# Kernel tuning notes

Hardware: AMD Instinct MI355X
Metric: run time of the kernel (lower is better)

## Reference

```python
import jax, jax.numpy as jnp
import numpy as np

H = 8          # num_heads
FOCUS = 3      # focusing_factor
EPS = 1e-6


def _disagreement(h):
    # h: [B, Hn, N, d]; mean of pairwise cosine-sim matrix with diagonal zeroed
    B, Hn, N, d = h.shape
    hn = h / jnp.maximum(jnp.linalg.norm(h, axis=-1, keepdims=True), 1e-12)
    sim_sum = jnp.sum(jnp.einsum('bhnd,bhmd->bhnm', hn, hn))
    diag_sum = jnp.sum(hn * hn)  # diagonal entries of the sim matrix
    return (sim_sum - diag_sum) / (B * Hn * N * N)


def setup_inputs() -> dict:
    key = jax.random.key(0)
    ks = jax.random.split(key, 10)
    B, N, C, K = 4, 1024, 512, 10
    s = 0.02
    return {
        'Q': jax.random.normal(ks[0], (B, N, C), jnp.float32),
        'adj_mat': jax.random.randint(ks[1], (B, N, K), 0, N),
        'Wq': jax.random.normal(ks[2], (C, C), jnp.float32) * s,
        'bq': jnp.zeros((C,), jnp.float32),
        'Wk': jax.random.normal(ks[3], (C, C), jnp.float32) * s,
        'bk': jnp.zeros((C,), jnp.float32),
        'Wv': jax.random.normal(ks[4], (C, C), jnp.float32) * s,
        'bv': jnp.zeros((C,), jnp.float32),
        'scale_p': jnp.zeros((1, 1, C), jnp.float32),  # torch init: zeros
        'Wconv': jax.random.normal(ks[5], (C, C, K + 1), jnp.float32) * s,
        'bconv': jnp.zeros((C,), jnp.float32),
        'W2': jax.random.normal(ks[6], (C, C), jnp.float32) * s,
        'b2': jnp.zeros((C,), jnp.float32),
        'ln_g': jnp.ones((C,), jnp.float32),
        'ln_b': jnp.zeros((C,), jnp.float32),
        'Wo': jax.random.normal(ks[7], (C, C), jnp.float32) * s,
        'bo': jnp.zeros((C,), jnp.float32),
    }


def _forward(Q, adj_mat, Wq, bq, Wk, bk, Wv, bv, scale_p, Wconv, bconv,
             W2, b2, ln_g, ln_b, Wo, bo):
    B, N, C = Q.shape
    d = C // H
    q = Q @ Wq + bq
    k = Q @ Wk + bk
    v = Q @ Wv + bv

    # LocalFeatureExtractor on v: gather K neighbors, conv over (channel, K+1) window
    neigh = v[jnp.arange(B)[:, None, None], adj_mat]          # [B,N,K,C]
    feats = jnp.concatenate([v[:, :, None, :], neigh], axis=2)  # [B,N,K+1,C]
    conv = jnp.einsum('bntc,oct->bno', feats, Wconv) + bconv   # full-window conv1d
    x_local = conv @ W2 + b2                                   # [B,N,C]

    # kernelized q/k with softplus scale and focused normalization
    q = jax.nn.relu(q) + EPS
    k = jax.nn.relu(k) + EPS
    scale = jax.nn.softplus(scale_p)
    q = q / scale
    k = k / scale

    def focus(x):
        n = jnp.linalg.norm(x, axis=-1, keepdims=True)
        return (x / (n + EPS)) ** FOCUS * n

    q = focus(q)
    k = focus(k)

    q = q.reshape(B, N, H, d).transpose(0, 2, 1, 3)
    k = k.reshape(B, N, H, d).transpose(0, 2, 1, 3)
    vh = v.reshape(B, N, H, d).transpose(0, 2, 1, 3)

    # linear attention: z normalization and kv summarization
    z = 1.0 / (jnp.einsum('bhnd,bhd->bhn', q, k.mean(axis=2)) + EPS)  # [B,H,N]
    kv = jnp.einsum('bhnd,bhne->bhde', k, vh) / N                     # [B,H,d,d]
    x = jnp.einsum('bhnd,bhde->bhne', q, kv) * z[..., None]           # [B,H,N,d]

    loss_local = _disagreement(vh)
    loss_kv = _disagreement(kv)

    x = x.transpose(0, 2, 1, 3).reshape(B, N, C) + x_local
    x4 = x.reshape(B, H, N, d)  # raw memory reinterpretation, matches torch .reshape
    loss_out = _disagreement(x4)
    loss = (loss_local + loss_out + loss_kv) / 3.0
    x = x4.reshape(B, N, C)

    # out_proj: LayerNorm then Linear
    mu = x.mean(axis=-1, keepdims=True)
    var = jnp.mean((x - mu) ** 2, axis=-1, keepdims=True)
    xn = (x - mu) / jnp.sqrt(var + 1e-5) * ln_g + ln_b
    out = xn @ Wo + bo
    return out, loss


def reference(Q, adj_mat, Wq, bq, Wk, bk, Wv, bv, scale_p, Wconv, bconv,
              W2, b2, ln_g, ln_b, Wo, bo):
    return _forward(Q, adj_mat, Wq, bq, Wk, bk, Wv, bv, scale_p, Wconv, bconv,
                    W2, b2, ln_g, ln_b, Wo, bo)
```

## Files before the change

### kernel.cpp

```cpp
#include <hip/hip_runtime.h>
#include <math.h>

#define TOK_TOTAL 4096
#define KNB 10
#define MATE 2097152

typedef __attribute__((ext_vector_type(8))) short short8;
typedef __attribute__((ext_vector_type(4))) float floatx4;
typedef unsigned short ushort;

__device__ __forceinline__ floatx4 mfma16(short8 a, short8 b, floatx4 c) {
  return __builtin_amdgcn_mfma_f32_16x16x32_bf16(a, b, c, 0, 0, 0);
}

__device__ __forceinline__ ushort f2bf(float f) {
  union { float f; unsigned int u; } x; x.f = f;
  unsigned int r = x.u + 0x7fffu + ((x.u >> 16) & 1u);
  return (ushort)(r >> 16);
}

__device__ __forceinline__ float bf2f(ushort u) {
  union { unsigned int u; float f; } x; x.u = ((unsigned int)u) << 16;
  return x.f;
}

__device__ __forceinline__ float lane_bcast(float v, int l) {
  union { float f; int i; } x; x.f = v;
  x.i = __builtin_amdgcn_readlane(x.i, l);
  return x.f;
}

__device__ __forceinline__ void glds16(const ushort* g, ushort* l) {
  __builtin_amdgcn_global_load_lds((const __attribute__((address_space(1))) void*)g,
                                   (__attribute__((address_space(3))) void*)l, 16, 0, 0);
}

__device__ __forceinline__ float wave_reduce_sum(float v) {
#pragma unroll
  for (int m = 32; m >= 1; m >>= 1) v += __shfl_xor(v, m, 64);
  return v;
}

__device__ __forceinline__ float block_reduce_sum_256(float v, float* red) {
  v = wave_reduce_sum(v);
  __syncthreads();
  if ((threadIdx.x & 63) == 0) red[threadIdx.x >> 6] = v;
  __syncthreads();
  return red[0] + red[1] + red[2] + red[3];
}

__global__ __launch_bounds__(256) void prep_kernel(const float* __restrict__ Wq,
                                                   const float* __restrict__ Wk,
                                                   const float* __restrict__ Wv,
                                                   const float* __restrict__ W2p,
                                                   const float* __restrict__ Wo,
                                                   const float* __restrict__ Wconv,
                                                   const float* __restrict__ Q,
                                                   const float* __restrict__ bq,
                                                   const float* __restrict__ bk,
                                                   const float* __restrict__ bv,
                                                   ushort* __restrict__ WT,
                                                   ushort* __restrict__ BcY,
                                                   float* __restrict__ biasqkv,
                                                   ushort* __restrict__ Qb) {
  int blk = blockIdx.x;
  if (blk < 1280) {
    __shared__ float tile[32][33];
    int zz = blk >> 8, rem = blk & 255;
    const float* W = (zz == 0) ? Wq : (zz == 1) ? Wk : (zz == 2) ? Wv
                     : (zz == 3) ? W2p : Wo;
    ushort* Wt = WT + (size_t)zz * 262144;
    int n0 = (rem & 15) * 32, k0 = (rem >> 4) * 32;
    int tx = threadIdx.x & 31, ty = threadIdx.x >> 5;
#pragma unroll
    for (int i = 0; i < 32; i += 8)
      tile[ty + i][tx] = W[(size_t)(k0 + ty + i) * 512 + n0 + tx];
    __syncthreads();
#pragma unroll
    for (int i = 0; i < 32; i += 8)
      Wt[(size_t)(n0 + ty + i) * 512 + k0 + tx] = f2bf(tile[tx][ty + i]);
  } else if (blk < 2304) {
    int i = (blk - 1280) * 256 + threadIdx.x;
    const float* src = Wconv + (size_t)i * 11;
    int o = i >> 9, c = i & 511;
#pragma unroll
    for (int t = 0; t < 11; ++t)
      BcY[(((size_t)(t * 512 + o)) << 9) + c] = f2bf(src[t]);
  } else if (blk == 2304) {
    for (int i = threadIdx.x; i < 1536; i += 256)
      biasqkv[i] = (i < 512) ? bq[i] : ((i < 1024) ? bk[i - 512] : bv[i - 1024]);
  } else {
    int i = (blk - 2305) * 256 + threadIdx.x;
    float4 v = *(const float4*)(Q + (size_t)i * 4);
    Qb[(size_t)i * 4 + 0] = f2bf(v.x);
    Qb[(size_t)i * 4 + 1] = f2bf(v.y);
    Qb[(size_t)i * 4 + 2] = f2bf(v.z);
    Qb[(size_t)i * 4 + 3] = f2bf(v.w);
  }
}

__global__ __launch_bounds__(256, 2) void gemm128(const ushort* __restrict__ A,
                                                  const ushort* __restrict__ Bt,
                                                  ushort* __restrict__ Cb,
                                                  int Ktot, int Ncols) {
  __shared__ __align__(16) ushort As[2][8192];
  __shared__ __align__(16) ushort Bs[2][8192];
  int tid = threadIdx.x, w = tid >> 6, lane = tid & 63;
  int lm = lane & 15, kq = lane >> 4;
  int row0 = blockIdx.y * 128, col0 = blockIdx.x * 128;
  int wm = w >> 1, wn = w & 1;

  bool isA = (w < 2);
  const ushort* gs[8];
  int go[8];
#pragma unroll
  for (int i = 0; i < 8; ++i) {
    int slab = (w & 1) * 4 + (i >> 1);
    int j = i & 1;
    const ushort* base = isA ? (A + (size_t)(row0 + slab * 16 + lm) * Ktot)
                             : (Bt + (size_t)(col0 + slab * 16 + lm) * Ktot);
    gs[i] = base + j * 32 + kq * 8;
    go[i] = slab * 1024 + j * 512;
  }

  floatx4 acc[4][4];
#pragma unroll
  for (int i = 0; i < 4; ++i)
#pragma unroll
    for (int j = 0; j < 4; ++j)
#pragma unroll
      for (int e = 0; e < 4; ++e) acc[i][j][e] = 0.f;

#pragma unroll
  for (int i = 0; i < 8; ++i)
    glds16(gs[i], (isA ? As[0] : Bs[0]) + go[i]);

  int nsteps = Ktot >> 6;
  for (int s = 0; s < nsteps; ++s) {
    int buf = s & 1;
    __syncthreads();
    if (s + 1 < nsteps) {
      int koff = (s + 1) << 6;
      ushort* dst = (isA ? As[buf ^ 1] : Bs[buf ^ 1]);
#pragma unroll
      for (int i = 0; i < 8; ++i) glds16(gs[i] + koff, dst + go[i]);
    }
#pragma unroll
    for (int j = 0; j < 2; ++j) {
      short8 a[4], b[4];
#pragma unroll
      for (int mt = 0; mt < 4; ++mt)
        a[mt] = *(const short8*)(&As[buf][(wm * 4 + mt) * 1024 + j * 512 + lane * 8]);
#pragma unroll
      for (int nt = 0; nt < 4; ++nt)
        b[nt] = *(const short8*)(&Bs[buf][(wn * 4 + nt) * 1024 + j * 512 + lane * 8]);
#pragma unroll
      for (int mt = 0; mt < 4; ++mt)
#pragma unroll
        for (int nt = 0; nt < 4; ++nt)
          acc[mt][nt] = mfma16(a[mt], b[nt], acc[mt][nt]);
    }
  }

#pragma unroll
  for (int mt = 0; mt < 4; ++mt) {
#pragma unroll
    for (int nt = 0; nt < 4; ++nt) {
      int col = col0 + wn * 64 + nt * 16 + lm;
#pragma unroll
      for (int r = 0; r < 4; ++r) {
        int row = row0 + wm * 64 + mt * 16 + kq * 4 + r;
        Cb[(size_t)row * Ncols + col] = f2bf(acc[mt][nt][r]);
      }
    }
  }
}

__global__ __launch_bounds__(256, 2) void gemm128_qkv(const ushort* __restrict__ A,
                                                      const ushort* __restrict__ Bt,
                                                      const float* __restrict__ bias,
                                                      float* __restrict__ outf,
                                                      ushort* __restrict__ vb) {
  __shared__ __align__(16) ushort As[2][8192];
  __shared__ __align__(16) ushort Bs[2][8192];
  int tid = threadIdx.x, w = tid >> 6, lane = tid & 63;
  int lm = lane & 15, kq = lane >> 4;
  int row0 = blockIdx.y * 128, col0 = blockIdx.x * 128;
  int wm = w >> 1, wn = w & 1;

  bool isA = (w < 2);
  const ushort* gs[8];
  int go[8];
#pragma unroll
  for (int i = 0; i < 8; ++i) {
    int slab = (w & 1) * 4 + (i >> 1);
    int j = i & 1;
    const ushort* base = isA ? (A + (size_t)(row0 + slab * 16 + lm) * 512)
                             : (Bt + (size_t)(col0 + slab * 16 + lm) * 512);
    gs[i] = base + j * 32 + kq * 8;
    go[i] = slab * 1024 + j * 512;
  }

  floatx4 acc[4][4];
#pragma unroll
  for (int i = 0; i < 4; ++i)
#pragma unroll
    for (int j = 0; j < 4; ++j)
#pragma unroll
      for (int e = 0; e < 4; ++e) acc[i][j][e] = 0.f;

#pragma unroll
  for (int i = 0; i < 8; ++i)
    glds16(gs[i], (isA ? As[0] : Bs[0]) + go[i]);

  for (int s = 0; s < 8; ++s) {
    int buf = s & 1;
    __syncthreads();
    if (s + 1 < 8) {
      int koff = (s + 1) << 6;
      ushort* dst = (isA ? As[buf ^ 1] : Bs[buf ^ 1]);
#pragma unroll
      for (int i = 0; i < 8; ++i) glds16(gs[i] + koff, dst + go[i]);
    }
#pragma unroll
    for (int j = 0; j < 2; ++j) {
      short8 a[4], b[4];
#pragma unroll
      for (int mt = 0; mt < 4; ++mt)
        a[mt] = *(const short8*)(&As[buf][(wm * 4 + mt) * 1024 + j * 512 + lane * 8]);
#pragma unroll
      for (int nt = 0; nt < 4; ++nt)
        b[nt] = *(const short8*)(&Bs[buf][(wn * 4 + nt) * 1024 + j * 512 + lane * 8]);
#pragma unroll
      for (int mt = 0; mt < 4; ++mt)
#pragma unroll
        for (int nt = 0; nt < 4; ++nt)
          acc[mt][nt] = mfma16(a[mt], b[nt], acc[mt][nt]);
    }
  }

#pragma unroll
  for (int mt = 0; mt < 4; ++mt) {
#pragma unroll
    for (int nt = 0; nt < 4; ++nt) {
      int col = col0 + wn * 64 + nt * 16 + lm;
      int mat = col >> 9, cc = col & 511;
      float bs = bias[col];
#pragma unroll
      for (int r = 0; r < 4; ++r) {
        int row = row0 + wm * 64 + mt * 16 + kq * 4 + r;
        float val = acc[mt][nt][r] + bs;
        size_t idx = (size_t)row * 512 + cc;
        outf[(size_t)mat * MATE + idx] = val;
        if (mat == 2) vb[idx] = f2bf(val);
      }
    }
  }
}

__global__ __launch_bounds__(256) void gather_add_bias(const ushort* __restrict__ Y,
                                                       const int* __restrict__ adj,
                                                       const float* __restrict__ bias,
                                                       ushort* __restrict__ convb) {
  int n = (blockIdx.x << 1) + (threadIdx.x >> 7);
  int b10 = (n >> 10) << 10;
  int o = (threadIdx.x & 127) << 2;
  float4 bs = *(const float4*)(bias + o);
  float a0 = bs.x, a1 = bs.y, a2 = bs.z, a3 = bs.w;
#pragma unroll
  for (int t = 0; t < 11; ++t) {
    int src = (t == 0) ? n : (b10 + adj[(size_t)n * KNB + (t - 1)]);
    const ushort* p = Y + (size_t)src * 5632 + (size_t)t * 512 + o;
    uint2 u = *(const uint2*)p;
    a0 += bf2f((ushort)(u.x & 0xffff));
    a1 += bf2f((ushort)(u.x >> 16));
    a2 += bf2f((ushort)(u.y & 0xffff));
    a3 += bf2f((ushort)(u.y >> 16));
  }
  uint2 w;
  w.x = (unsigned)f2bf(a0) | ((unsigned)f2bf(a1) << 16);
  w.y = (unsigned)f2bf(a2) | ((unsigned)f2bf(a3) << 16);
  *(uint2*)(convb + (size_t)n * 512 + o) = w;
}

__global__ __launch_bounds__(256) void gather_add(const ushort* __restrict__ Y,
                                                  const int* __restrict__ adj,
                                                  float* __restrict__ convf,
                                                  int t0, int ntaps, int ncols) {
  int n = blockIdx.x;
  int b10 = (n >> 10) << 10;
  int o = threadIdx.x * 2;
  float a0 = 0.f, a1 = 0.f;
  for (int t = t0; t < t0 + ntaps; ++t) {
    int src = (t == 0) ? n : (b10 + adj[(size_t)n * KNB + (t - 1)]);
    const ushort* p = Y + (size_t)src * ncols + (size_t)(t - t0) * 512 + o;
    a0 += bf2f(p[0]);
    a1 += bf2f(p[1]);
  }
  convf[(size_t)n * 512 + o] += a0;
  convf[(size_t)n * 512 + o + 1] += a1;
}

__global__ __launch_bounds__(256) void convbias_cast(const float* __restrict__ cf,
                                                     const float* __restrict__ bias,
                                                     ushort* __restrict__ cb) {
  int i = blockIdx.x * 256 + threadIdx.x;
  float4 v = *(const float4*)(cf + (size_t)i * 4);
  int c = (i * 4) & 511;
  cb[(size_t)i * 4 + 0] = f2bf(v.x + bias[c + 0]);
  cb[(size_t)i * 4 + 1] = f2bf(v.y + bias[c + 1]);
  cb[(size_t)i * 4 + 2] = f2bf(v.z + bias[c + 2]);
  cb[(size_t)i * 4 + 3] = f2bf(v.w + bias[c + 3]);
}

__global__ __launch_bounds__(256) void gemm64(const ushort* __restrict__ A,
                                              const ushort* __restrict__ Bt,
                                              const float* __restrict__ bias,
                                              float* __restrict__ Cf,
                                              ushort* __restrict__ Cb,
                                              int Ktot) {
  __shared__ __align__(16) ushort As[2][4096];
  __shared__ __align__(16) ushort Bs[2][4096];
  int tid = threadIdx.x, w = tid >> 6, lane = tid & 63;
  int lm = lane & 15, kq = lane >> 4;
  int row0 = blockIdx.y * 64, col0 = blockIdx.x * 64;
  int wm = w >> 1, wn = w & 1;

  const ushort* gsrc[4];
  int goff[4];
  bool isA = (w < 2);
#pragma unroll
  for (int i = 0; i < 4; ++i) {
    int l = w * 4 + i, t, j;
    const ushort* base;
    if (l < 8) { t = l >> 1; j = l & 1; base = A + (size_t)(row0 + t * 16 + lm) * Ktot; }
    else { int lb = l - 8; t = lb >> 1; j = lb & 1; base = Bt + (size_t)(col0 + t * 16 + lm) * Ktot; }
    gsrc[i] = base + j * 32 + kq * 8;
    goff[i] = t * 1024 + j * 512;
  }

  floatx4 acc[2][2];
#pragma unroll
  for (int i = 0; i < 2; ++i)
#pragma unroll
    for (int j = 0; j < 2; ++j)
#pragma unroll
      for (int e = 0; e < 4; ++e) acc[i][j][e] = 0.f;

#pragma unroll
  for (int i = 0; i < 4; ++i)
    glds16(gsrc[i], (isA ? As[0] : Bs[0]) + goff[i]);

  int nsteps = Ktot >> 6;
  for (int s = 0; s < nsteps; ++s) {
    int buf = s & 1;
    __syncthreads();
    if (s + 1 < nsteps) {
      int koff = (s + 1) << 6;
      ushort* dst = (isA ? As[buf ^ 1] : Bs[buf ^ 1]);
#pragma unroll
      for (int i = 0; i < 4; ++i) glds16(gsrc[i] + koff, dst + goff[i]);
    }
#pragma unroll
    for (int j = 0; j < 2; ++j) {
      short8 a0 = *(const short8*)(&As[buf][(wm * 2 + 0) * 1024 + j * 512 + lane * 8]);
      short8 a1 = *(const short8*)(&As[buf][(wm * 2 + 1) * 1024 + j * 512 + lane * 8]);
      short8 b0 = *(const short8*)(&Bs[buf][(wn * 2 + 0) * 1024 + j * 512 + lane * 8]);
      short8 b1 = *(const short8*)(&Bs[buf][(wn * 2 + 1) * 1024 + j * 512 + lane * 8]);
      acc[0][0] = mfma16(a0, b0, acc[0][0]);
      acc[0][1] = mfma16(a0, b1, acc[0][1]);
      acc[1][0] = mfma16(a1, b0, acc[1][0]);
      acc[1][1] = mfma16(a1, b1, acc[1][1]);
    }
  }

  int colb = col0 + wn * 32;
  int rowb = row0 + wm * 32 + kq * 4;
#pragma unroll
  for (int mt = 0; mt < 2; ++mt) {
#pragma unroll
    for (int nt = 0; nt < 2; ++nt) {
      int col = colb + nt * 16 + lm;
      float bs = bias[col];
#pragma unroll
      for (int r = 0; r < 4; ++r) {
        int row = rowb + mt * 16 + r;
        float val = acc[mt][nt][r] + bs;
        size_t idx = (size_t)row * 512 + col;
        if (Cf) Cf[idx] = val;
        if (Cb) Cb[idx] = f2bf(val);
      }
    }
  }
}

__global__ __launch_bounds__(256) void focus_kernel(float* __restrict__ x,
                                                    const float* __restrict__ scale_p) {
  __shared__ float red[4];
  int row = blockIdx.x;
  float* p = x + (size_t)row * 512;
  int tid = threadIdx.x;
  float sp0 = scale_p[tid], sp1 = scale_p[tid + 256];
  float sc0 = sp0 > 20.f ? sp0 : log1pf(expf(sp0));
  float sc1 = sp1 > 20.f ? sp1 : log1pf(expf(sp1));
  float v0 = (fmaxf(p[tid], 0.f) + 1e-6f) / sc0;
  float v1 = (fmaxf(p[tid + 256], 0.f) + 1e-6f) / sc1;
  float tot = block_reduce_sum_256(v0 * v0 + v1 * v1, red);
  float n = sqrtf(tot);
  float np = n + 1e-6f;
  float f = n / (np * np * np);
  p[tid] = v0 * v0 * v0 * f;
  p[tid + 256] = v1 * v1 * v1 * f;
}

__global__ __launch_bounds__(256) void kv_kernel(const float* __restrict__ kf,
                                                 const float* __restrict__ v,
                                                 float* __restrict__ kv,
                                                 float* __restrict__ Sacc,
                                                 float* __restrict__ Dacc,
                                                 float* __restrict__ kmean) {
  __shared__ float Ks[16][64];
  __shared__ float Vs[16][64];
  __shared__ float Spart[64];
  __shared__ float Kpart[64];
  __shared__ float Dpart;
  int bh = blockIdx.x >> 3, chunk = blockIdx.x & 7;
  int b = bh >> 3, h = bh & 7;
  int tid = threadIdx.x;
  int lr = tid >> 4, lc = (tid & 15) << 2;
  int tx = tid & 15, ty = tid >> 4;
  if (tid < 64) { Spart[tid] = 0.f; Kpart[tid] = 0.f; }
  if (tid == 0) Dpart = 0.f;
  __syncthreads();
  const float* kbase = kf + (size_t)b * 524288 + h * 64 + (size_t)chunk * 128 * 512;
  const float* vbase = v + (size_t)b * 524288 + h * 64 + (size_t)chunk * 128 * 512;
  float acc[4][4] = {};
  float Sloc[4] = {0.f, 0.f, 0.f, 0.f};
  float Kloc[4] = {0.f, 0.f, 0.f, 0.f};
  float Dloc = 0.f;
  for (int n0 = 0; n0 < 128; n0 += 16) {
    float4 ke = *(const float4*)(kbase + (size_t)(n0 + lr) * 512 + lc);
    *(float4*)(&Ks[lr][lc]) = ke;
    Kloc[0] += ke.x; Kloc[1] += ke.y; Kloc[2] += ke.z; Kloc[3] += ke.w;
    float4 ve = *(const float4*)(vbase + (size_t)(n0 + lr) * 512 + lc);
    *(float4*)(&Vs[lr][lc]) = ve;
    __syncthreads();
    float sq = ve.x * ve.x + ve.y * ve.y + ve.z * ve.z + ve.w * ve.w;
#pragma unroll
    for (int m = 1; m < 16; m <<= 1) sq += __shfl_xor(sq, m, 64);
    float cn = fmaxf(sqrtf(sq), 1e-12f);
    Sloc[0] += ve.x / cn; Sloc[1] += ve.y / cn;
    Sloc[2] += ve.z / cn; Sloc[3] += ve.w / cn;
    if ((tid & 15) == 0) Dloc += sq / (cn * cn);
#pragma unroll
    for (int kk = 0; kk < 16; ++kk) {
      float a[4], bb[4];
#pragma unroll
      for (int i = 0; i < 4; ++i) a[i] = Ks[kk][ty * 4 + i];
#pragma unroll
      for (int j = 0; j < 4; ++j) bb[j] = Vs[kk][tx * 4 + j];
#pragma unroll
      for (int i = 0; i < 4; ++i)
#pragma unroll
        for (int j = 0; j < 4; ++j) acc[i][j] += a[i] * bb[j];
    }
    __syncthreads();
  }
#pragma unroll
  for (int i = 0; i < 4; ++i)
#pragma unroll
    for (int j = 0; j < 4; ++j)
      atomicAdd(&kv[(size_t)bh * 4096 + (ty * 4 + i) * 64 + tx * 4 + j],
                acc[i][j] * (1.f / 1024.f));
#pragma unroll
  for (int i = 0; i < 4; ++i) {
    atomicAdd(&Spart[lc + i], Sloc[i]);
    atomicAdd(&Kpart[lc + i], Kloc[i]);
  }
  if ((tid & 15) == 0) atomicAdd(&Dpart, Dloc);
  __syncthreads();
  if (tid < 64) {
    atomicAdd(&Sacc[bh * 64 + tid], Spart[tid]);
    atomicAdd(&kmean[b * 512 + h * 64 + tid], Kpart[tid] * (1.f / 1024.f));
  }
  if (tid == 64) atomicAdd(&Dacc[bh], Dpart);
}

__global__ __launch_bounds__(512, 4) void attn_ln_kernel(const float* __restrict__ qf,
                                                         const float* __restrict__ kvf,
                                                         const float* __restrict__ kmean,
                                                         const float* __restrict__ x_local,
                                                         const float* __restrict__ g,
                                                         const float* __restrict__ bp,
                                                         ushort* __restrict__ xn,
                                                         float* __restrict__ Sacc,
                                                         float* __restrict__ Dacc,
                                                         float* __restrict__ Skv,
                                                         float* __restrict__ Dkv) {
  __shared__ __align__(16) ushort kvs[32768];
  __shared__ float red[16];
  __shared__ float Sl[8][64];
  __shared__ float Dl[8];
  int r0 = blockIdx.x << 3;
  int b = r0 >> 10;
  int c = threadIdx.x, wv = c >> 6, lane = c & 63;
  const float4* kvg = (const float4*)(kvf + (size_t)b * 32768);
#pragma unroll
  for (int i = 0; i < 16; ++i) {
    float4 kvv = kvg[c + i * 512];
    int o = (c + i * 512) << 2;
    kvs[o + 0] = f2bf(kvv.x); kvs[o + 1] = f2bf(kvv.y);
    kvs[o + 2] = f2bf(kvv.z); kvs[o + 3] = f2bf(kvv.w);
  }
  float kmr = kmean[b * 512 + c];
  float gr = g[c], bpr = bp[c];
  __syncthreads();
  unsigned int kvr[32];
#pragma unroll
  for (int i = 0; i < 32; ++i) {
    unsigned int lo = kvs[wv * 4096 + (2 * i) * 64 + lane];
    unsigned int hi = kvs[wv * 4096 + (2 * i + 1) * 64 + lane];
    kvr[i] = lo | (hi << 16);
  }
  float Sreg = 0.f, Dreg = 0.f;
  for (int r = 0; r < 8; ++r) {
    int row = r0 + r;
    float qv = qf[(size_t)row * 512 + c];
    float xl = x_local[(size_t)row * 512 + c];
    float zd = wave_reduce_sum(qv * kmr);
    float zz = 1.f / (zd + 1e-6f);
    float s = 0.f;
#pragma unroll
    for (int i = 0; i < 32; ++i) {
      union { unsigned int u; float f; } lo, hi;
      lo.u = kvr[i] << 16;
      hi.u = kvr[i] & 0xffff0000u;
      s += lane_bcast(qv, 2 * i) * lo.f;
      s += lane_bcast(qv, 2 * i + 1) * hi.f;
    }
    float xv = s * zz + xl;
    float s1 = wave_reduce_sum(xv);
    float s2 = wave_reduce_sum(xv * xv);
    if (lane == 0) { red[wv] = s1; red[8 + wv] = s2; }
    __syncthreads();
    float tsum = red[0] + red[1] + red[2] + red[3] + red[4] + red[5] + red[6] + red[7];
    float tsq = red[8] + red[9] + red[10] + red[11] + red[12] + red[13] + red[14] + red[15];
    __syncthreads();
    float mu = tsum * (1.f / 512.f);
    float var = tsq * (1.f / 512.f) - mu * mu;
    float inv = rsqrtf(fmaxf(var, 0.f) + 1e-5f);
    xn[(size_t)row * 512 + c] = f2bf((xv - mu) * inv * gr + bpr);
    float norm = fmaxf(sqrtf(s2), 1e-12f);
    Sreg += xv / norm;
    Dreg += s2 / (norm * norm);
  }
  Sl[wv][lane] = Sreg;
  if (lane == 0) Dl[wv] = Dreg;
  __syncthreads();
  int gx = b * 8 + ((r0 & 1023) >> 7);
  if (c < 64) {
    float ssum = 0.f;
#pragma unroll
    for (int ww = 0; ww < 8; ++ww) ssum += Sl[ww][c];
    atomicAdd(&Sacc[gx * 64 + c], ssum);
  } else if (c == 64) {
    float dsum = 0.f;
#pragma unroll
    for (int ww = 0; ww < 8; ++ww) dsum += Dl[ww];
    atomicAdd(&Dacc[gx], dsum);
  }
  if ((blockIdx.x & 127) == 0) {
    float S2 = 0.f, D2 = 0.f;
#pragma unroll
    for (int i = 0; i < 32; ++i) {
      union { unsigned int u; float f; } lo, hi;
      lo.u = kvr[i] << 16;
      hi.u = kvr[i] & 0xffff0000u;
      float sq = wave_reduce_sum(lo.f * lo.f);
      float nrm = fmaxf(sqrtf(sq), 1e-12f);
      float hn = lo.f / nrm;
      S2 += hn; D2 += hn * hn;
      sq = wave_reduce_sum(hi.f * hi.f);
      nrm = fmaxf(sqrtf(sq), 1e-12f);
      hn = hi.f / nrm;
      S2 += hn; D2 += hn * hn;
    }
    float dt = wave_reduce_sum(D2);
    atomicAdd(&Skv[(b * 8 + wv) * 64 + lane], S2);
    if (lane == 0) atomicAdd(&Dkv[b * 8 + wv], dt);
  }
}

__global__ __launch_bounds__(64) void disagree_final_all(const float* __restrict__ Sall,
                                                         const float* __restrict__ Dall,
                                                         float s0, float s1, float s2,
                                                         float* __restrict__ loss) {
  int set = blockIdx.x >> 5, gg = blockIdx.x & 31;
  int l = threadIdx.x;
  float sv = Sall[set * 2048 + gg * 64 + l];
  float sim = wave_reduce_sum(sv * sv);
  if (l == 0) {
    float scale = (set == 0) ? s0 : (set == 1) ? s1 : s2;
    atomicAdd(loss, (sim - Dall[set * 32 + gg]) * scale);
  }
}

extern "C" void kernel_launch(void* const* d_in, const int* in_sizes, int n_in,
                              void* d_out, int out_size, void* d_ws, size_t ws_size,
                              hipStream_t stream) {
  const float* Q       = (const float*)d_in[0];
  const int*   adj     = (const int*)d_in[1];
  const float* Wq      = (const float*)d_in[2];
  const float* bq      = (const float*)d_in[3];
  const float* Wk      = (const float*)d_in[4];
  const float* bk      = (const float*)d_in[5];
  const float* Wv      = (const float*)d_in[6];
  const float* bv      = (const float*)d_in[7];
  const float* scale_p = (const float*)d_in[8];
  const float* Wconv   = (const float*)d_in[9];
  const float* bconv   = (const float*)d_in[10];
  const float* W2      = (const float*)d_in[11];
  const float* b2      = (const float*)d_in[12];
  const float* ln_g    = (const float*)d_in[13];
  const float* ln_b    = (const float*)d_in[14];
  const float* Wo      = (const float*)d_in[15];
  const float* bo      = (const float*)d_in[16];

  float* out = (float*)d_out;
  float* loss_slot = out + MATE;

  float* ws = (float*)d_ws;
  float* q0      = ws;
  float* k0      = q0 + MATE;
  float* v       = k0 + MATE;
  float* x_local = v + MATE;
  float* convf   = x_local + MATE;
  ushort* Qb    = (ushort*)(convf + MATE);
  ushort* vb    = Qb + MATE;
  ushort* convb = vb + MATE;
  ushort* xnb   = convb + MATE;
  ushort* WqT   = xnb + MATE;
  ushort* W2T   = WqT + 3 * 262144;
  ushort* WoT   = W2T + 262144;
  ushort* BcY   = WoT + 262144;
  float* biasqkv = (float*)(BcY + 5632 * 512);
  float* kmean = biasqkv + 1536;
  float* kvbuf = kmean + 2048;
  float* Sv    = kvbuf + 131072;
  float* Skv   = Sv + 2048;
  float* Sx    = Skv + 2048;
  float* Dv    = Sx + 2048;
  float* Dkv   = Dv + 32;
  float* Dx    = Dkv + 32;
  float* ytail = Dx + 32;
  ushort* Ybf  = (ushort*)ytail;

  size_t used_floats = (size_t)(ytail - ws);
  size_t avail_floats = (ws_size / 4 > used_floats) ? (ws_size / 4 - used_floats) : 0;
  int TC = (int)(avail_floats / (MATE / 2));
  if (TC < 1) TC = 1;
  if (TC > 11) TC = 11;

  hipMemsetAsync(loss_slot, 0, sizeof(float), stream);
  hipMemsetAsync(kmean, 0, (2048 + 131072 + 3 * 2048 + 96) * sizeof(float), stream);

  prep_kernel<<<4353, 256, 0, stream>>>(Wq, Wk, Wv, W2, Wo, Wconv, Q,
                                        bq, bk, bv, WqT, BcY, biasqkv, Qb);

  gemm128_qkv<<<dim3(12, 32), 256, 0, stream>>>(Qb, WqT, biasqkv, q0, vb);

  if (TC >= 11) {
    gemm128<<<dim3(44, 32), 256, 0, stream>>>(vb, BcY, Ybf, 512, 5632);
    gather_add_bias<<<2048, 256, 0, stream>>>(Ybf, adj, bconv, convb);
  } else {
    hipMemsetAsync(convf, 0, MATE * sizeof(float), stream);
    for (int t0 = 0; t0 < 11; t0 += TC) {
      int nt = (11 - t0 < TC) ? (11 - t0) : TC;
      int ncols = nt * 512;
      gemm128<<<dim3(ncols / 128, 32), 256, 0, stream>>>(
          vb, BcY + (size_t)(t0 * 512) * 512, Ybf, 512, ncols);
      gather_add<<<4096, 256, 0, stream>>>(Ybf, adj, convf, t0, nt, ncols);
    }
    convbias_cast<<<2048, 256, 0, stream>>>(convf, bconv, convb);
  }

  gemm64<<<dim3(8, 64), 256, 0, stream>>>(convb, W2T, b2, x_local, nullptr, 512);

  focus_kernel<<<2 * TOK_TOTAL, 256, 0, stream>>>(q0, scale_p);

  kv_kernel<<<256, 256, 0, stream>>>(k0, v, kvbuf, Sv, Dv, kmean);

  attn_ln_kernel<<<512, 512, 0, stream>>>(q0, kvbuf, kmean, x_local,
                                          ln_g, ln_b, xnb, Sx, Dx, Skv, Dkv);

  disagree_final_all<<<96, 64, 0, stream>>>(Sv, Dv,
                                            1.f / (33554432.f * 3.f),
                                            1.f / (131072.f * 3.f),
                                            1.f / (33554432.f * 3.f), loss_slot);

  gemm64<<<dim3(8, 64), 256, 0, stream>>>(xnb, WoT, bo, out, nullptr, 512);
}
```

Measured before the change: 295.8 us.

## Fold W2 into conv weights and fuse neighbor gather into a split-K GEMM

```diff
diff --git a/kernel.cpp b/kernel.cpp
--- a/kernel.cpp
+++ b/kernel.cpp
@@ -17,11 +17,6 @@
   union { float f; unsigned int u; } x; x.f = f;
   unsigned int r = x.u + 0x7fffu + ((x.u >> 16) & 1u);
   return (ushort)(r >> 16);
-}
-
-__device__ __forceinline__ float bf2f(ushort u) {
-  union { unsigned int u; float f; } x; x.u = ((unsigned int)u) << 16;
-  return x.f;
 }
 
 __device__ __forceinline__ float lane_bcast(float v, int l) {
@@ -59,9 +54,12 @@
                                                    const float* __restrict__ bq,
                                                    const float* __restrict__ bk,
                                                    const float* __restrict__ bv,
+                                                   const float* __restrict__ bconv,
+                                                   const float* __restrict__ b2,
                                                    ushort* __restrict__ WT,
-                                                   ushort* __restrict__ BcY,
+                                                   ushort* __restrict__ WcT,
                                                    float* __restrict__ biasqkv,
+                                                   float* __restrict__ bias2f,
                                                    ushort* __restrict__ Qb) {
   int blk = blockIdx.x;
   if (blk < 1280) {
@@ -81,16 +79,27 @@
       Wt[(size_t)(n0 + ty + i) * 512 + k0 + tx] = f2bf(tile[tx][ty + i]);
   } else if (blk < 2304) {
     int i = (blk - 1280) * 256 + threadIdx.x;
-    const float* src = Wconv + (size_t)i * 11;
-    int o = i >> 9, c = i & 511;
+    int o1 = i & 511, c = i >> 9;
+    const float* src = Wconv + ((size_t)o1 * 512 + c) * 11;
 #pragma unroll
     for (int t = 0; t < 11; ++t)
-      BcY[(((size_t)(t * 512 + o)) << 9) + c] = f2bf(src[t]);
+      WcT[(((size_t)(t * 512 + c)) << 9) + o1] = f2bf(src[t]);
   } else if (blk == 2304) {
     for (int i = threadIdx.x; i < 1536; i += 256)
       biasqkv[i] = (i < 512) ? bq[i] : ((i < 1024) ? bk[i - 512] : bv[i - 1024]);
+  } else if (blk < 2307) {
+    __shared__ float bc[512];
+    int tid = threadIdx.x;
+    bc[tid] = bconv[tid];
+    bc[tid + 256] = bconv[tid + 256];
+    __syncthreads();
+    int o = (blk - 2305) * 256 + tid;
+    float s = b2[o];
+#pragma unroll 4
+    for (int o1 = 0; o1 < 512; ++o1) s += bc[o1] * W2p[(size_t)o1 * 512 + o];
+    bias2f[o] = s;
   } else {
-    int i = (blk - 2305) * 256 + threadIdx.x;
+    int i = (blk - 2307) * 256 + threadIdx.x;
     float4 v = *(const float4*)(Q + (size_t)i * 4);
     Qb[(size_t)i * 4 + 0] = f2bf(v.x);
     Qb[(size_t)i * 4 + 1] = f2bf(v.y);
@@ -258,59 +267,127 @@
   }
 }
 
-__global__ __launch_bounds__(256) void gather_add_bias(const ushort* __restrict__ Y,
-                                                       const int* __restrict__ adj,
-                                                       const float* __restrict__ bias,
-                                                       ushort* __restrict__ convb) {
-  int n = (blockIdx.x << 1) + (threadIdx.x >> 7);
-  int b10 = (n >> 10) << 10;
-  int o = (threadIdx.x & 127) << 2;
-  float4 bs = *(const float4*)(bias + o);
-  float a0 = bs.x, a1 = bs.y, a2 = bs.z, a3 = bs.w;
-#pragma unroll
-  for (int t = 0; t < 11; ++t) {
-    int src = (t == 0) ? n : (b10 + adj[(size_t)n * KNB + (t - 1)]);
-    const ushort* p = Y + (size_t)src * 5632 + (size_t)t * 512 + o;
-    uint2 u = *(const uint2*)p;
-    a0 += bf2f((ushort)(u.x & 0xffff));
-    a1 += bf2f((ushort)(u.x >> 16));
-    a2 += bf2f((ushort)(u.y & 0xffff));
-    a3 += bf2f((ushort)(u.y >> 16));
-  }
-  uint2 w;
-  w.x = (unsigned)f2bf(a0) | ((unsigned)f2bf(a1) << 16);
-  w.y = (unsigned)f2bf(a2) | ((unsigned)f2bf(a3) << 16);
-  *(uint2*)(convb + (size_t)n * 512 + o) = w;
-}
-
-__global__ __launch_bounds__(256) void gather_add(const ushort* __restrict__ Y,
-                                                  const int* __restrict__ adj,
-                                                  float* __restrict__ convf,
-                                                  int t0, int ntaps, int ncols) {
-  int n = blockIdx.x;
-  int b10 = (n >> 10) << 10;
-  int o = threadIdx.x * 2;
-  float a0 = 0.f, a1 = 0.f;
-  for (int t = t0; t < t0 + ntaps; ++t) {
-    int src = (t == 0) ? n : (b10 + adj[(size_t)n * KNB + (t - 1)]);
-    const ushort* p = Y + (size_t)src * ncols + (size_t)(t - t0) * 512 + o;
-    a0 += bf2f(p[0]);
-    a1 += bf2f(p[1]);
-  }
-  convf[(size_t)n * 512 + o] += a0;
-  convf[(size_t)n * 512 + o + 1] += a1;
-}
-
-__global__ __launch_bounds__(256) void convbias_cast(const float* __restrict__ cf,
-                                                     const float* __restrict__ bias,
-                                                     ushort* __restrict__ cb) {
-  int i = blockIdx.x * 256 + threadIdx.x;
-  float4 v = *(const float4*)(cf + (size_t)i * 4);
-  int c = (i * 4) & 511;
-  cb[(size_t)i * 4 + 0] = f2bf(v.x + bias[c + 0]);
-  cb[(size_t)i * 4 + 1] = f2bf(v.y + bias[c + 1]);
-  cb[(size_t)i * 4 + 2] = f2bf(v.z + bias[c + 2]);
-  cb[(size_t)i * 4 + 3] = f2bf(v.w + bias[c + 3]);
+__global__ __launch_bounds__(256) void gemm_gather(const ushort* __restrict__ A,
+                                                   const ushort* __restrict__ Bt,
+                                                   const int* __restrict__ adj,
+                                                   const float* __restrict__ bias2,
+                                                   float* __restrict__ xpart) {
+  __shared__ __align__(16) ushort As[2][8192];
+  __shared__ __align__(16) ushort Bs[2][8192];
+  int tid = threadIdx.x, w = tid >> 6, lane = tid & 63;
+  int lm = lane & 15, kq = lane >> 4;
+  int row0 = blockIdx.y * 128, col0 = blockIdx.x * 128;
+  int z = blockIdx.z;
+  int kbase = z * 2816;
+  int wm = w >> 1, wn = w & 1;
+  bool isA = (w < 2);
+
+  int go[8];
+#pragma unroll
+  for (int i = 0; i < 8; ++i) {
+    int slab = (w & 1) * 4 + (i >> 1);
+    go[i] = slab * 1024 + (i & 1) * 512;
+  }
+
+  int rowi[4], b10v[4], srcnext[4];
+  const ushort* gsB[8];
+  if (isA) {
+    int tap0 = kbase >> 9;
+    int t0 = tap0 ? tap0 : 1;
+#pragma unroll
+    for (int p = 0; p < 4; ++p) {
+      int r = row0 + ((w & 1) * 4 + p) * 16 + lm;
+      rowi[p] = r;
+      b10v[p] = (r >> 10) << 10;
+      int av = b10v[p] + adj[r * KNB + t0 - 1];
+      srcnext[p] = tap0 ? av : r;
+    }
+  } else {
+#pragma unroll
+    for (int i = 0; i < 8; ++i) {
+      int slab = (w & 1) * 4 + (i >> 1);
+      gsB[i] = Bt + (size_t)(col0 + slab * 16 + lm) * 5632 + kbase + (i & 1) * 32 + kq * 8;
+    }
+  }
+
+  floatx4 acc[4][4];
+#pragma unroll
+  for (int i = 0; i < 4; ++i)
+#pragma unroll
+    for (int j = 0; j < 4; ++j)
+#pragma unroll
+      for (int e = 0; e < 4; ++e) acc[i][j][e] = 0.f;
+
+  {
+    int koff = kbase & 511;
+    if (isA) {
+#pragma unroll
+      for (int i = 0; i < 8; ++i)
+        glds16(A + (size_t)srcnext[i >> 1] * 512 + koff + (i & 1) * 32 + kq * 8,
+               As[0] + go[i]);
+    } else {
+#pragma unroll
+      for (int i = 0; i < 8; ++i) glds16(gsB[i], Bs[0] + go[i]);
+    }
+  }
+
+  const int nsteps = 44;
+  for (int s = 0; s < nsteps; ++s) {
+    int buf = s & 1;
+    __syncthreads();
+    if (s + 1 < nsteps) {
+      if (isA) {
+        int koff = (kbase + (s + 1) * 64) & 511;
+        ushort* dst = As[buf ^ 1];
+#pragma unroll
+        for (int i = 0; i < 8; ++i)
+          glds16(A + (size_t)srcnext[i >> 1] * 512 + koff + (i & 1) * 32 + kq * 8,
+                 dst + go[i]);
+        int s2 = (s + 2 < nsteps) ? s + 2 : nsteps - 1;
+        int tap2 = (kbase + s2 * 64) >> 9;
+        int t2 = tap2 ? tap2 : 1;
+#pragma unroll
+        for (int p = 0; p < 4; ++p) {
+          int av = b10v[p] + adj[rowi[p] * KNB + t2 - 1];
+          srcnext[p] = tap2 ? av : rowi[p];
+        }
+      } else {
+        ushort* dst = Bs[buf ^ 1];
+#pragma unroll
+        for (int i = 0; i < 8; ++i) glds16(gsB[i] + (s + 1) * 64, dst + go[i]);
+      }
+    }
+#pragma unroll
+    for (int j = 0; j < 2; ++j) {
+      short8 a[4], b[4];
+#pragma unroll
+      for (int mt = 0; mt < 4; ++mt)
+        a[mt] = *(const short8*)(&As[buf][(wm * 4 + mt) * 1024 + j * 512 + lane * 8]);
+#pragma unroll
+      for (int nt = 0; nt < 4; ++nt)
+        b[nt] = *(const short8*)(&Bs[buf][(wn * 4 + nt) * 1024 + j * 512 + lane * 8]);
+#pragma unroll
+      for (int mt = 0; mt < 4; ++mt)
+#pragma unroll
+        for (int nt = 0; nt < 4; ++nt)
+          acc[mt][nt] = mfma16(a[mt], b[nt], acc[mt][nt]);
+    }
+  }
+
+  float* outp = xpart + (size_t)z * MATE;
+#pragma unroll
+  for (int mt = 0; mt < 4; ++mt) {
+#pragma unroll
+    for (int nt = 0; nt < 4; ++nt) {
+      int col = col0 + wn * 64 + nt * 16 + lm;
+      float bs = (z == 0) ? bias2[col] : 0.f;
+#pragma unroll
+      for (int r = 0; r < 4; ++r) {
+        int row = row0 + wm * 64 + mt * 16 + kq * 4 + r;
+        outp[(size_t)row * 512 + col] = acc[mt][nt][r] + bs;
+      }
+    }
+  }
 }
 
 __global__ __launch_bounds__(256) void gemm64(const ushort* __restrict__ A,
@@ -526,7 +603,7 @@
   for (int r = 0; r < 8; ++r) {
     int row = r0 + r;
     float qv = qf[(size_t)row * 512 + c];
-    float xl = x_local[(size_t)row * 512 + c];
+    float xl = x_local[(size_t)row * 512 + c] + x_local[(size_t)MATE + (size_t)row * 512 + c];
     float zd = wave_reduce_sum(qv * kmr);
     float zz = 1.f / (zd + 1e-6f);
     float s = 0.f;
@@ -633,18 +710,17 @@
   float* q0      = ws;
   float* k0      = q0 + MATE;
   float* v       = k0 + MATE;
-  float* x_local = v + MATE;
-  float* convf   = x_local + MATE;
-  ushort* Qb    = (ushort*)(convf + MATE);
+  float* xpart   = v + MATE;
+  ushort* Qb    = (ushort*)(xpart + 2 * MATE);
   ushort* vb    = Qb + MATE;
-  ushort* convb = vb + MATE;
-  ushort* xnb   = convb + MATE;
+  ushort* xnb   = vb + MATE;
   ushort* WqT   = xnb + MATE;
   ushort* W2T   = WqT + 3 * 262144;
   ushort* WoT   = W2T + 262144;
-  ushort* BcY   = WoT + 262144;
-  float* biasqkv = (float*)(BcY + 5632 * 512);
-  float* kmean = biasqkv + 1536;
+  ushort* WcT   = WoT + 262144;
+  float* biasqkv = (float*)(WcT + (size_t)5632 * 512);
+  float* bias2f = biasqkv + 1536;
+  float* kmean = bias2f + 512;
   float* kvbuf = kmean + 2048;
   float* Sv    = kvbuf + 131072;
   float* Skv   = Sv + 2048;
@@ -652,45 +728,26 @@
   float* Dv    = Sx + 2048;
   float* Dkv   = Dv + 32;
   float* Dx    = Dkv + 32;
-  float* ytail = Dx + 32;
-  ushort* Ybf  = (ushort*)ytail;
-
-  size_t used_floats = (size_t)(ytail - ws);
-  size_t avail_floats = (ws_size / 4 > used_floats) ? (ws_size / 4 - used_floats) : 0;
-  int TC = (int)(avail_floats / (MATE / 2));
-  if (TC < 1) TC = 1;
-  if (TC > 11) TC = 11;
+  ushort* Bt2  = (ushort*)(Dx + 32);
 
   hipMemsetAsync(loss_slot, 0, sizeof(float), stream);
   hipMemsetAsync(kmean, 0, (2048 + 131072 + 3 * 2048 + 96) * sizeof(float), stream);
 
-  prep_kernel<<<4353, 256, 0, stream>>>(Wq, Wk, Wv, W2, Wo, Wconv, Q,
-                                        bq, bk, bv, WqT, BcY, biasqkv, Qb);
+  prep_kernel<<<4355, 256, 0, stream>>>(Wq, Wk, Wv, W2, Wo, Wconv, Q,
+                                        bq, bk, bv, bconv, b2,
+                                        WqT, WcT, biasqkv, bias2f, Qb);
+
+  gemm128<<<dim3(44, 4), 256, 0, stream>>>(W2T, WcT, Bt2, 512, 5632);
 
   gemm128_qkv<<<dim3(12, 32), 256, 0, stream>>>(Qb, WqT, biasqkv, q0, vb);
 
-  if (TC >= 11) {
-    gemm128<<<dim3(44, 32), 256, 0, stream>>>(vb, BcY, Ybf, 512, 5632);
-    gather_add_bias<<<2048, 256, 0, stream>>>(Ybf, adj, bconv, convb);
-  } else {
-    hipMemsetAsync(convf, 0, MATE * sizeof(float), stream);
-    for (int t0 = 0; t0 < 11; t0 += TC) {
-      int nt = (11 - t0 < TC) ? (11 - t0) : TC;
-      int ncols = nt * 512;
-      gemm128<<<dim3(ncols / 128, 32), 256, 0, stream>>>(
-          vb, BcY + (size_t)(t0 * 512) * 512, Ybf, 512, ncols);
-      gather_add<<<4096, 256, 0, stream>>>(Ybf, adj, convf, t0, nt, ncols);
-    }
-    convbias_cast<<<2048, 256, 0, stream>>>(convf, bconv, convb);
-  }
-
-  gemm64<<<dim3(8, 64), 256, 0, stream>>>(convb, W2T, b2, x_local, nullptr, 512);
+  gemm_gather<<<dim3(4, 32, 2), 256, 0, stream>>>(vb, Bt2, adj, bias2f, xpart);
 
   focus_kernel<<<2 * TOK_TOTAL, 256, 0, stream>>>(q0, scale_p);
 
   kv_kernel<<<256, 256, 0, stream>>>(k0, v, kvbuf, Sv, Dv, kmean);
 
-  attn_ln_kernel<<<512, 512, 0, stream>>>(q0, kvbuf, kmean, x_local,
+  attn_ln_kernel<<<512, 512, 0, stream>>>(q0, kvbuf, kmean, xpart,
                                           ln_g, ln_b, xnb, Sx, Dx, Skv, Dkv);
 
   disagree_final_all<<<96, 64, 0, stream>>>(Sv, Dv,
```

Measured after the change: 365.2 us. +23.5%, slower.
